# Optimization experiments

Measured on AMD Instinct MI355X. Metric: run time of the kernel, lower is better.

## Reference

```python
import jax, jax.numpy as jnp
import numpy as np

EMBED = 256
HEADS = 8
GROUP = 64
HEAD_DIM = EMBED // HEADS
N = 131072

def setup_inputs() -> dict:
    key = jax.random.key(0)
    k1, k2, k3 = jax.random.split(key, 3)
    s_in = 1.0 / np.sqrt(EMBED)
    x = jax.random.normal(k1, (N, EMBED), dtype=jnp.float32)
    w_qkv = jax.random.normal(k2, (3 * EMBED, EMBED), dtype=jnp.float32) * s_in  # nn.Linear weight [out,in]
    w_out = jax.random.normal(k3, (EMBED, EMBED), dtype=jnp.float32) * s_in
    b_out = jnp.zeros((EMBED,), dtype=jnp.float32)
    return {"x": x, "w_qkv": w_qkv, "w_out": w_out, "b_out": b_out}

def reference(x, w_qkv, w_out, b_out):
    Ntok, C = x.shape
    ng = Ntok // GROUP  # number of groups
    qkv = x @ w_qkv.T                      # (N, 3C)
    qkv = qkv.reshape(Ntok, 3, C)
    q, k, v = qkv[:, 0], qkv[:, 1], qkv[:, 2]

    def to_heads(t):
        # '(n g) (h c) -> (n h) g c'
        t = t.reshape(ng, GROUP, HEADS, HEAD_DIM)
        return t.transpose(0, 2, 1, 3).reshape(ng * HEADS, GROUP, HEAD_DIM)

    q, k, v = to_heads(q), to_heads(k), to_heads(v)
    # grouped attention over local windows of size GROUP
    energy = jnp.einsum('nqd,nkd->nqk', q, k)           # (n*h, g, g)
    attn = jax.nn.softmax(energy / jnp.sqrt(jnp.float32(C)), axis=-1)  # scale by sqrt(embed_size), as in source
    out = jnp.einsum('nql,nld->nqd', attn, v)           # (n*h, g, hd)
    # '(n h) g c -> (n g) (h c)'
    out = out.reshape(ng, HEADS, GROUP, HEAD_DIM).transpose(0, 2, 1, 3).reshape(Ntok, C)
    return out @ w_out.T + b_out
```

## Files before the change

### kernel.cpp

```cpp
#include <hip/hip_runtime.h>
#include <hip/hip_bf16.h>
#include <stdint.h>

typedef __attribute__((ext_vector_type(8))) short s16x8;
typedef __attribute__((ext_vector_type(4))) float f32x4;

__device__ __forceinline__ unsigned short f32_bf16(float f) {
  union { float f; uint32_t u; } v; v.f = f;
  return (unsigned short)((v.u + 0x7FFFu + ((v.u >> 16) & 1u)) >> 16);
}

__device__ __forceinline__ uint32_t pack_bf16(float lo, float hi) {
  __hip_bfloat162 h = __float22bfloat162_rn(float2{lo, hi});
  union { __hip_bfloat162 h; uint32_t u; } u; u.h = h; return u.u;
}

__device__ __forceinline__ s16x8 xchg(uint32_t lo0, uint32_t lo1,
                                      uint32_t hi0, uint32_t hi1,
                                      int srcA, int srcB, uint32_t hisel) {
  int a0 = __shfl((int)lo0, srcA), b0 = __shfl((int)hi0, srcA);
  int a1 = __shfl((int)lo1, srcA), b1 = __shfl((int)hi1, srcA);
  int a2 = __shfl((int)lo0, srcB), b2 = __shfl((int)hi0, srcB);
  int a3 = __shfl((int)lo1, srcB), b3 = __shfl((int)hi1, srcB);
  union { uint32_t u[4]; s16x8 v; } r;
  r.u[0] = hisel ? (uint32_t)b0 : (uint32_t)a0;
  r.u[1] = hisel ? (uint32_t)b1 : (uint32_t)a1;
  r.u[2] = hisel ? (uint32_t)b2 : (uint32_t)a2;
  r.u[3] = hisel ? (uint32_t)b3 : (uint32_t)a3;
  return r.v;
}

__global__ void convert_w(const float* __restrict__ wqkv,
                          const float* __restrict__ wout,
                          unsigned short* __restrict__ o) {
  int i = blockIdx.x * 256 + threadIdx.x;
  if (i < 768 * 256) o[i] = f32_bf16(wqkv[i]);
  else               o[i] = f32_bf16(wout[i - 768 * 256]);
}

__global__ __launch_bounds__(512, 4) void qkv_attn(
    const float* __restrict__ x,
    const unsigned short* __restrict__ wqkv,
    unsigned short* __restrict__ aout) {
  __shared__ unsigned short xt[64 * 256];

  const int g    = blockIdx.x;
  const int tid  = threadIdx.x;
  const int h    = tid >> 6;
  const int lane = tid & 63;
  const int l15  = lane & 15;
  const int l4   = lane >> 4;

  {
    const int row = tid >> 3;
    const int c0  = (tid & 7) * 32;
    const float* src = x + (size_t)(g * 64 + row) * 256 + c0;
    const uint32_t swz = (uint32_t)(row & 7) << 4;
#pragma unroll
    for (int c = 0; c < 32; c += 8) {
      float4 f0 = *(const float4*)(src + c);
      float4 f1 = *(const float4*)(src + c + 4);
      uint32_t p0 = pack_bf16(f0.x, f0.y);
      uint32_t p1 = pack_bf16(f0.z, f0.w);
      uint32_t p2 = pack_bf16(f1.x, f1.y);
      uint32_t p3 = pack_bf16(f1.z, f1.w);
      uint32_t byte = ((uint32_t)(row * 512 + (c0 + c) * 2)) ^ swz;
      *(uint4*)((char*)xt + byte) = make_uint4(p0, p1, p2, p3);
    }
  }
  __syncthreads();

  const uint32_t swz   = (uint32_t)(l15 & 7) << 4;
  const int      srcA  = l15 + ((lane & 16) << 1);
  const int      srcB  = srcA + 16;
  const uint32_t hisel = (uint32_t)(lane & 32);

  const unsigned short* wbase = wqkv + (size_t)(h * 32 + l15) * 256 + l4 * 8;

  f32x4 qT[2][4], kT[2][4];
#pragma unroll
  for (int t = 0; t < 2; ++t)
#pragma unroll
    for (int m = 0; m < 4; ++m) {
      qT[t][m] = (f32x4){0.f, 0.f, 0.f, 0.f};
      kT[t][m] = (f32x4){0.f, 0.f, 0.f, 0.f};
    }

  for (int kk = 0; kk < 8; ++kk) {
    s16x8 a[4];
#pragma unroll
    for (int m = 0; m < 4; ++m) {
      uint32_t byte = ((uint32_t)((16 * m + l15) * 512 + kk * 64 + l4 * 16)) ^ swz;
      a[m] = *(const s16x8*)((const char*)xt + byte);
    }
#pragma unroll
    for (int t = 0; t < 2; ++t) {
      const unsigned short* wp = wbase + (size_t)(16 * t) * 256 + kk * 32;
      s16x8 wq = *(const s16x8*)(wp);
      s16x8 wk = *(const s16x8*)(wp + 256 * 256);
#pragma unroll
      for (int m = 0; m < 4; ++m) {
        qT[t][m] = __builtin_amdgcn_mfma_f32_16x16x32_bf16(wq, a[m], qT[t][m], 0, 0, 0);
        kT[t][m] = __builtin_amdgcn_mfma_f32_16x16x32_bf16(wk, a[m], kT[t][m], 0, 0, 0);
      }
    }
  }

  s16x8 kA[4], qB[4];
#pragma unroll
  for (int m = 0; m < 4; ++m) {
    uint32_t q00 = pack_bf16(qT[0][m][0], qT[0][m][1]);
    uint32_t q01 = pack_bf16(qT[0][m][2], qT[0][m][3]);
    uint32_t q10 = pack_bf16(qT[1][m][0], qT[1][m][1]);
    uint32_t q11 = pack_bf16(qT[1][m][2], qT[1][m][3]);
    qB[m] = xchg(q00, q01, q10, q11, srcA, srcB, hisel);
    uint32_t k00 = pack_bf16(kT[0][m][0], kT[0][m][1]);
    uint32_t k01 = pack_bf16(kT[0][m][2], kT[0][m][3]);
    uint32_t k10 = pack_bf16(kT[1][m][0], kT[1][m][1]);
    uint32_t k11 = pack_bf16(kT[1][m][2], kT[1][m][3]);
    kA[m] = xchg(k00, k01, k10, k11, srcA, srcB, hisel);
  }

  f32x4 e[4][4];
#pragma unroll
  for (int m = 0; m < 4; ++m)
#pragma unroll
    for (int n = 0; n < 4; ++n) {
      e[m][n] = (f32x4){0.f, 0.f, 0.f, 0.f};
      e[m][n] = __builtin_amdgcn_mfma_f32_16x16x32_bf16(kA[m], qB[n], e[m][n], 0, 0, 0);
    }

  uint32_t pkP[4][4][2];
#pragma unroll
  for (int n = 0; n < 4; ++n) {
    float mx = e[0][n][0];
#pragma unroll
    for (int m = 0; m < 4; ++m)
#pragma unroll
      for (int r = 0; r < 4; ++r) mx = fmaxf(mx, e[m][n][r]);
    mx = fmaxf(mx, __shfl_xor(mx, 16));
    mx = fmaxf(mx, __shfl_xor(mx, 32));
    float p[4][4];
    float sum = 0.f;
#pragma unroll
    for (int m = 0; m < 4; ++m)
#pragma unroll
      for (int r = 0; r < 4; ++r) {
        float t = __expf((e[m][n][r] - mx) * 0.0625f);
        p[m][r] = t;
        sum += t;
      }
    sum += __shfl_xor(sum, 16);
    sum += __shfl_xor(sum, 32);
    float rs = 1.0f / sum;
#pragma unroll
    for (int m = 0; m < 4; ++m) {
      pkP[n][m][0] = pack_bf16(p[m][0] * rs, p[m][1] * rs);
      pkP[n][m][1] = pack_bf16(p[m][2] * rs, p[m][3] * rs);
    }
  }

  f32x4 vv[4][2];
#pragma unroll
  for (int m = 0; m < 4; ++m) {
    vv[m][0] = (f32x4){0.f, 0.f, 0.f, 0.f};
    vv[m][1] = (f32x4){0.f, 0.f, 0.f, 0.f};
  }
  for (int kk = 0; kk < 8; ++kk) {
    s16x8 a[4];
#pragma unroll
    for (int m = 0; m < 4; ++m) {
      uint32_t byte = ((uint32_t)((16 * m + l15) * 512 + kk * 64 + l4 * 16)) ^ swz;
      a[m] = *(const s16x8*)((const char*)xt + byte);
    }
    const unsigned short* wp = wbase + (size_t)512 * 256 + kk * 32;
    s16x8 wv0 = *(const s16x8*)(wp);
    s16x8 wv1 = *(const s16x8*)(wp + 16 * 256);
#pragma unroll
    for (int m = 0; m < 4; ++m) {
      vv[m][0] = __builtin_amdgcn_mfma_f32_16x16x32_bf16(a[m], wv0, vv[m][0], 0, 0, 0);
      vv[m][1] = __builtin_amdgcn_mfma_f32_16x16x32_bf16(a[m], wv1, vv[m][1], 0, 0, 0);
    }
  }
  uint32_t pkV[2][4][2];
#pragma unroll
  for (int t = 0; t < 2; ++t)
#pragma unroll
    for (int m = 0; m < 4; ++m) {
      pkV[t][m][0] = pack_bf16(vv[m][t][0], vv[m][t][1]);
      pkV[t][m][1] = pack_bf16(vv[m][t][2], vv[m][t][3]);
    }

  f32x4 o[4][2];
#pragma unroll
  for (int nb = 0; nb < 4; ++nb) {
    o[nb][0] = (f32x4){0.f, 0.f, 0.f, 0.f};
    o[nb][1] = (f32x4){0.f, 0.f, 0.f, 0.f};
  }
#pragma unroll
  for (int kk2 = 0; kk2 < 2; ++kk2) {
    s16x8 vB[2];
#pragma unroll
    for (int t = 0; t < 2; ++t)
      vB[t] = xchg(pkV[t][2 * kk2][0], pkV[t][2 * kk2][1],
                   pkV[t][2 * kk2 + 1][0], pkV[t][2 * kk2 + 1][1], srcA, srcB, hisel);
#pragma unroll
    for (int nb = 0; nb < 4; ++nb) {
      s16x8 pA = xchg(pkP[nb][2 * kk2][0], pkP[nb][2 * kk2][1],
                      pkP[nb][2 * kk2 + 1][0], pkP[nb][2 * kk2 + 1][1], srcA, srcB, hisel);
      o[nb][0] = __builtin_amdgcn_mfma_f32_16x16x32_bf16(pA, vB[0], o[nb][0], 0, 0, 0);
      o[nb][1] = __builtin_amdgcn_mfma_f32_16x16x32_bf16(pA, vB[1], o[nb][1], 0, 0, 0);
    }
  }

  unsigned short* dst = aout + (size_t)g * 64 * 256 + h * 32;
#pragma unroll
  for (int nb = 0; nb < 4; ++nb)
#pragma unroll
    for (int t = 0; t < 2; ++t)
#pragma unroll
      for (int r = 0; r < 4; ++r)
        dst[(size_t)(16 * nb + 4 * l4 + r) * 256 + 16 * t + l15] = f32_bf16(o[nb][t][r]);
}

__global__ __launch_bounds__(256) void proj(
    const unsigned short* __restrict__ A,
    const unsigned short* __restrict__ Bw,
    const float* __restrict__ bias,
    float* __restrict__ out) {
  __shared__ unsigned short As[128 * 64];
  __shared__ unsigned short Bs[128 * 64];
  const int bm = blockIdx.x, bn = blockIdx.y;
  const int tid = threadIdx.x;
  const int w = tid >> 6, lane = tid & 63;
  const int l15 = lane & 15, l4 = lane >> 4;
  const int wr = w >> 1, wc = w & 1;

  f32x4 acc[4][4];
#pragma unroll
  for (int mi = 0; mi < 4; ++mi)
#pragma unroll
    for (int ni = 0; ni < 4; ++ni) acc[mi][ni] = (f32x4){0.f, 0.f, 0.f, 0.f};

  const int srow = tid >> 1;
  const int sc0  = (tid & 1) * 32;
  const unsigned short* ga = A  + (size_t)(bm * 128 + srow) * 256 + sc0;
  const unsigned short* gb = Bw + (size_t)(bn * 128 + srow) * 256 + sc0;

  for (int kk = 0; kk < 4; ++kk) {
#pragma unroll
    for (int c = 0; c < 32; c += 8) {
      uint4 va = *(const uint4*)(ga + kk * 64 + c);
      uint4 vb = *(const uint4*)(gb + kk * 64 + c);
      uint32_t byte = (uint32_t)(srow * 128 + (sc0 + c) * 2) ^ ((srow & 7) << 4);
      *(uint4*)((char*)As + byte) = va;
      *(uint4*)((char*)Bs + byte) = vb;
    }
    __syncthreads();
#pragma unroll
    for (int k2 = 0; k2 < 2; ++k2) {
      s16x8 af[4], bf[4];
#pragma unroll
      for (int mi = 0; mi < 4; ++mi) {
        int row = wr * 64 + 16 * mi + l15;
        uint32_t byte = (uint32_t)(row * 128 + k2 * 64 + l4 * 16) ^ ((row & 7) << 4);
        af[mi] = *(const s16x8*)((const char*)As + byte);
      }
#pragma unroll
      for (int ni = 0; ni < 4; ++ni) {
        int row = wc * 64 + 16 * ni + l15;
        uint32_t byte = (uint32_t)(row * 128 + k2 * 64 + l4 * 16) ^ ((row & 7) << 4);
        bf[ni] = *(const s16x8*)((const char*)Bs + byte);
      }
#pragma unroll
      for (int mi = 0; mi < 4; ++mi)
#pragma unroll
        for (int ni = 0; ni < 4; ++ni)
          acc[mi][ni] = __builtin_amdgcn_mfma_f32_16x16x32_bf16(af[mi], bf[ni], acc[mi][ni], 0, 0, 0);
    }
    __syncthreads();
  }

#pragma unroll
  for (int mi = 0; mi < 4; ++mi)
#pragma unroll
    for (int ni = 0; ni < 4; ++ni) {
      int col = bn * 128 + wc * 64 + 16 * ni + l15;
      float b = bias[col];
#pragma unroll
      for (int r = 0; r < 4; ++r) {
        int row = bm * 128 + wr * 64 + 16 * mi + l4 * 4 + r;
        out[(size_t)row * 256 + col] = acc[mi][ni][r] + b;
      }
    }
}

extern "C" void kernel_launch(void* const* d_in, const int* in_sizes, int n_in,
                              void* d_out, int out_size, void* d_ws, size_t ws_size,
                              hipStream_t stream) {
  const float* x    = (const float*)d_in[0];
  const float* wqkv = (const float*)d_in[1];
  const float* wout = (const float*)d_in[2];
  const float* bout = (const float*)d_in[3];
  float* out = (float*)d_out;

  unsigned short* wq_bf = (unsigned short*)d_ws;
  unsigned short* wo_bf = wq_bf + 768 * 256;
  unsigned short* aout  = wo_bf + 256 * 256;

  convert_w<<<1024, 256, 0, stream>>>(wqkv, wout, wq_bf);
  qkv_attn<<<2048, 512, 0, stream>>>(x, wq_bf, aout);
  proj<<<dim3(1024, 2), 256, 0, stream>>>(aout, wo_bf, bout, out);
}
```

Before: 257.0 us.

## Fuse output projection into attention kernel via shared-memory staging

Attention output is now written as bf16 into the existing shared tile instead of a global buffer, and each wave computes its 32 output columns of the projection directly from that tile, with W_out fragments read from global memory. This drops the separate projection kernel and the global round trip of the intermediate activations. The energy computation is also split per query block to shorten live ranges, and the occupancy hint drops from 4 to 2 blocks per unit, which may reduce latency hiding. Each block now re-reads all of W_out from global or cache.

New measurement: 209.1 us. 18.6% less time.

```diff
diff --git a/kernel.cpp b/kernel.cpp
--- a/kernel.cpp
+++ b/kernel.cpp
@@ -38,10 +38,12 @@
   else               o[i] = f32_bf16(wout[i - 768 * 256]);
 }
 
-__global__ __launch_bounds__(512, 4) void qkv_attn(
+__global__ __launch_bounds__(512, 2) void mha_fused(
     const float* __restrict__ x,
     const unsigned short* __restrict__ wqkv,
-    unsigned short* __restrict__ aout) {
+    const unsigned short* __restrict__ wout,
+    const float* __restrict__ bias,
+    float* __restrict__ out) {
   __shared__ unsigned short xt[64 * 256];
 
   const int g    = blockIdx.x;
@@ -121,23 +123,20 @@
     kA[m] = xchg(k00, k01, k10, k11, srcA, srcB, hisel);
   }
 
-  f32x4 e[4][4];
-#pragma unroll
-  for (int m = 0; m < 4; ++m)
-#pragma unroll
-    for (int n = 0; n < 4; ++n) {
-      e[m][n] = (f32x4){0.f, 0.f, 0.f, 0.f};
-      e[m][n] = __builtin_amdgcn_mfma_f32_16x16x32_bf16(kA[m], qB[n], e[m][n], 0, 0, 0);
-    }
-
   uint32_t pkP[4][4][2];
 #pragma unroll
   for (int n = 0; n < 4; ++n) {
-    float mx = e[0][n][0];
+    f32x4 en[4];
+#pragma unroll
+    for (int m = 0; m < 4; ++m) {
+      en[m] = (f32x4){0.f, 0.f, 0.f, 0.f};
+      en[m] = __builtin_amdgcn_mfma_f32_16x16x32_bf16(kA[m], qB[n], en[m], 0, 0, 0);
+    }
+    float mx = en[0][0];
 #pragma unroll
     for (int m = 0; m < 4; ++m)
 #pragma unroll
-      for (int r = 0; r < 4; ++r) mx = fmaxf(mx, e[m][n][r]);
+      for (int r = 0; r < 4; ++r) mx = fmaxf(mx, en[m][r]);
     mx = fmaxf(mx, __shfl_xor(mx, 16));
     mx = fmaxf(mx, __shfl_xor(mx, 32));
     float p[4][4];
@@ -146,7 +145,7 @@
     for (int m = 0; m < 4; ++m)
 #pragma unroll
       for (int r = 0; r < 4; ++r) {
-        float t = __expf((e[m][n][r] - mx) * 0.0625f);
+        float t = __expf((en[m][r] - mx) * 0.0625f);
         p[m][r] = t;
         sum += t;
       }
@@ -213,85 +212,53 @@
     }
   }
 
-  unsigned short* dst = aout + (size_t)g * 64 * 256 + h * 32;
+  __syncthreads();
 #pragma unroll
   for (int nb = 0; nb < 4; ++nb)
 #pragma unroll
     for (int t = 0; t < 2; ++t)
 #pragma unroll
-      for (int r = 0; r < 4; ++r)
-        dst[(size_t)(16 * nb + 4 * l4 + r) * 256 + 16 * t + l15] = f32_bf16(o[nb][t][r]);
-}
-
-__global__ __launch_bounds__(256) void proj(
-    const unsigned short* __restrict__ A,
-    const unsigned short* __restrict__ Bw,
-    const float* __restrict__ bias,
-    float* __restrict__ out) {
-  __shared__ unsigned short As[128 * 64];
-  __shared__ unsigned short Bs[128 * 64];
-  const int bm = blockIdx.x, bn = blockIdx.y;
-  const int tid = threadIdx.x;
-  const int w = tid >> 6, lane = tid & 63;
-  const int l15 = lane & 15, l4 = lane >> 4;
-  const int wr = w >> 1, wc = w & 1;
-
-  f32x4 acc[4][4];
-#pragma unroll
-  for (int mi = 0; mi < 4; ++mi)
-#pragma unroll
-    for (int ni = 0; ni < 4; ++ni) acc[mi][ni] = (f32x4){0.f, 0.f, 0.f, 0.f};
-
-  const int srow = tid >> 1;
-  const int sc0  = (tid & 1) * 32;
-  const unsigned short* ga = A  + (size_t)(bm * 128 + srow) * 256 + sc0;
-  const unsigned short* gb = Bw + (size_t)(bn * 128 + srow) * 256 + sc0;
-
-  for (int kk = 0; kk < 4; ++kk) {
-#pragma unroll
-    for (int c = 0; c < 32; c += 8) {
-      uint4 va = *(const uint4*)(ga + kk * 64 + c);
-      uint4 vb = *(const uint4*)(gb + kk * 64 + c);
-      uint32_t byte = (uint32_t)(srow * 128 + (sc0 + c) * 2) ^ ((srow & 7) << 4);
-      *(uint4*)((char*)As + byte) = va;
-      *(uint4*)((char*)Bs + byte) = vb;
-    }
-    __syncthreads();
-#pragma unroll
-    for (int k2 = 0; k2 < 2; ++k2) {
-      s16x8 af[4], bf[4];
-#pragma unroll
-      for (int mi = 0; mi < 4; ++mi) {
-        int row = wr * 64 + 16 * mi + l15;
-        uint32_t byte = (uint32_t)(row * 128 + k2 * 64 + l4 * 16) ^ ((row & 7) << 4);
-        af[mi] = *(const s16x8*)((const char*)As + byte);
+      for (int r = 0; r < 4; ++r) {
+        int row = 16 * nb + 4 * l4 + r;
+        int col = h * 32 + 16 * t + l15;
+        uint32_t byte = ((uint32_t)(row * 512 + col * 2)) ^ ((uint32_t)(row & 7) << 4);
+        *(unsigned short*)((char*)xt + byte) = f32_bf16(o[nb][t][r]);
       }
-#pragma unroll
-      for (int ni = 0; ni < 4; ++ni) {
-        int row = wc * 64 + 16 * ni + l15;
-        uint32_t byte = (uint32_t)(row * 128 + k2 * 64 + l4 * 16) ^ ((row & 7) << 4);
-        bf[ni] = *(const s16x8*)((const char*)Bs + byte);
-      }
-#pragma unroll
-      for (int mi = 0; mi < 4; ++mi)
-#pragma unroll
-        for (int ni = 0; ni < 4; ++ni)
-          acc[mi][ni] = __builtin_amdgcn_mfma_f32_16x16x32_bf16(af[mi], bf[ni], acc[mi][ni], 0, 0, 0);
-    }
-    __syncthreads();
-  }
-
-#pragma unroll
-  for (int mi = 0; mi < 4; ++mi)
-#pragma unroll
-    for (int ni = 0; ni < 4; ++ni) {
-      int col = bn * 128 + wc * 64 + 16 * ni + l15;
-      float b = bias[col];
-#pragma unroll
-      for (int r = 0; r < 4; ++r) {
-        int row = bm * 128 + wr * 64 + 16 * mi + l4 * 4 + r;
-        out[(size_t)row * 256 + col] = acc[mi][ni][r] + b;
-      }
+  __syncthreads();
+
+  f32x4 acc[4][2];
+#pragma unroll
+  for (int m = 0; m < 4; ++m) {
+    acc[m][0] = (f32x4){0.f, 0.f, 0.f, 0.f};
+    acc[m][1] = (f32x4){0.f, 0.f, 0.f, 0.f};
+  }
+  const unsigned short* wobase = wout + (size_t)(h * 32 + l15) * 256 + l4 * 8;
+  for (int kk = 0; kk < 8; ++kk) {
+    s16x8 a[4];
+#pragma unroll
+    for (int m = 0; m < 4; ++m) {
+      uint32_t byte = ((uint32_t)((16 * m + l15) * 512 + kk * 64 + l4 * 16)) ^ swz;
+      a[m] = *(const s16x8*)((const char*)xt + byte);
+    }
+    s16x8 wo0 = *(const s16x8*)(wobase + kk * 32);
+    s16x8 wo1 = *(const s16x8*)(wobase + (size_t)16 * 256 + kk * 32);
+#pragma unroll
+    for (int m = 0; m < 4; ++m) {
+      acc[m][0] = __builtin_amdgcn_mfma_f32_16x16x32_bf16(a[m], wo0, acc[m][0], 0, 0, 0);
+      acc[m][1] = __builtin_amdgcn_mfma_f32_16x16x32_bf16(a[m], wo1, acc[m][1], 0, 0, 0);
+    }
+  }
+
+  const float b0 = bias[h * 32 + l15];
+  const float b1 = bias[h * 32 + 16 + l15];
+  float* dst = out + (size_t)g * 64 * 256 + h * 32;
+#pragma unroll
+  for (int m = 0; m < 4; ++m)
+#pragma unroll
+    for (int r = 0; r < 4; ++r) {
+      int tok = 16 * m + 4 * l4 + r;
+      dst[(size_t)tok * 256 + l15]      = acc[m][0][r] + b0;
+      dst[(size_t)tok * 256 + 16 + l15] = acc[m][1][r] + b1;
     }
 }
 
@@ -306,9 +273,7 @@
 
   unsigned short* wq_bf = (unsigned short*)d_ws;
   unsigned short* wo_bf = wq_bf + 768 * 256;
-  unsigned short* aout  = wo_bf + 256 * 256;
 
   convert_w<<<1024, 256, 0, stream>>>(wqkv, wout, wq_bf);
-  qkv_attn<<<2048, 512, 0, stream>>>(x, wq_bf, aout);
-  proj<<<dim3(1024, 2), 256, 0, stream>>>(aout, wo_bf, bout, out);
-}
+  mha_fused<<<2048, 512, 0, stream>>>(x, wq_bf, wo_bf, bout, out);
+}
```
